# Optimization experiments

Hardware: AMD Instinct MI355X
Metric: run time of the kernel (lower is better)

Reference implementation:

```python
import jax, jax.numpy as jnp
import numpy as np

DIM = 1024
HEADS = 16
HEAD_DIM = DIM // HEADS
B, N = 4, 4096


def setup_inputs() -> dict:
    key = jax.random.key(0)
    ks = jax.random.split(key, 10)
    s = 1.0 / np.sqrt(DIM)
    return {
        "x": jax.random.normal(ks[0], (B, N, DIM), dtype=jnp.float32),
        "Wq": jax.random.uniform(ks[1], (DIM, DIM), jnp.float32, -s, s),
        "bq": jax.random.uniform(ks[2], (DIM,), jnp.float32, -s, s),
        "Wk": jax.random.uniform(ks[3], (DIM, DIM), jnp.float32, -s, s),
        "bk": jax.random.uniform(ks[4], (DIM,), jnp.float32, -s, s),
        "Wv": jax.random.uniform(ks[5], (DIM, DIM), jnp.float32, -s, s),
        "bv": jax.random.uniform(ks[6], (DIM,), jnp.float32, -s, s),
        "Wo": jax.random.uniform(ks[7], (DIM, DIM), jnp.float32, -s, s),
        "bo": jax.random.uniform(ks[8], (DIM,), jnp.float32, -s, s),
        "stdp": jnp.ones((HEADS,), dtype=jnp.float32),
    }


def reference(x, Wq, bq, Wk, bk, Wv, bv, Wo, bo, stdp):
    b, n, d = x.shape
    h, dh = HEADS, HEAD_DIM
    # projections (torch Linear: x @ W.T + b)
    def proj(W, bias):
        return (x @ W.T + bias).reshape(b, n, h, dh).transpose(0, 2, 1, 3)  # bhnd
    Q = jax.nn.elu(proj(Wq, bq)) + 1.0
    K = jax.nn.elu(proj(Wk, bk)) + 1.0
    V = proj(Wv, bv)
    stdp_w = jax.nn.sigmoid(stdp).reshape(1, h, 1, 1)
    KV = jnp.einsum('bhnd,bhnv->bhdv', K, V)      # (b,h,dh,dh)
    K_sum = K.sum(axis=2)                          # (b,h,dh)
    numerator = jnp.einsum('bhnd,bhdv->bhnv', Q, KV)
    denominator = jnp.einsum('bhnd,bhd->bhn', Q, K_sum)[..., None] + 1e-6
    attn_out = numerator / denominator * stdp_w    # (b,h,n,dh)
    out = attn_out.transpose(0, 2, 1, 3).reshape(b, n, d)
    out = out @ Wo.T + bo
    return (out, jax.lax.stop_gradient(stdp))
```

## Files before the change

### kernel.cpp

```cpp
#include <hip/hip_runtime.h>
#include <hip/hip_bf16.h>

#define DIMSZ 1024
#define SEQLEN 4096
#define NHEAD 16
#define NX 16777216L
#define NW 1048576L

typedef __attribute__((ext_vector_type(8))) short bf16x8;
typedef __attribute__((ext_vector_type(4))) float f32x4;

__device__ __forceinline__ unsigned short f2bf(float f) {
    union { float f; unsigned int i; } c; c.f = f;
    unsigned int x = c.i;
    unsigned int r = (x + 0x7fffu + ((x >> 16) & 1u)) >> 16;
    return (unsigned short)r;
}

__device__ __forceinline__ unsigned int pk2(float lo, float hi) {
    union { float f; unsigned int i; } a, b; a.f = lo; b.f = hi;
    return __builtin_amdgcn_perm(b.i + 0x8000u, a.i + 0x8000u, 0x07060302u);
}

__device__ __forceinline__ void unp8(const unsigned short* p, float* f) {
    uint4 w = *(const uint4*)p;
    union { unsigned int i; float f; } c;
    c.i = w.x << 16;           f[0] = c.f;
    c.i = w.x & 0xffff0000u;   f[1] = c.f;
    c.i = w.y << 16;           f[2] = c.f;
    c.i = w.y & 0xffff0000u;   f[3] = c.f;
    c.i = w.z << 16;           f[4] = c.f;
    c.i = w.z & 0xffff0000u;   f[5] = c.f;
    c.i = w.w << 16;           f[6] = c.f;
    c.i = w.w & 0xffff0000u;   f[7] = c.f;
}

__device__ __forceinline__ void unp8r(bf16x8 v, float* f) {
    union { bf16x8 s; uint4 w; } u; u.s = v;
    union { unsigned int i; float f; } c;
    c.i = u.w.x << 16;           f[0] = c.f;
    c.i = u.w.x & 0xffff0000u;   f[1] = c.f;
    c.i = u.w.y << 16;           f[2] = c.f;
    c.i = u.w.y & 0xffff0000u;   f[3] = c.f;
    c.i = u.w.z << 16;           f[4] = c.f;
    c.i = u.w.z & 0xffff0000u;   f[5] = c.f;
    c.i = u.w.w << 16;           f[6] = c.f;
    c.i = u.w.w & 0xffff0000u;   f[7] = c.f;
}

__device__ __forceinline__ void async16(const void* g, void* l) {
    __builtin_amdgcn_global_load_lds(
        (const __attribute__((address_space(1))) void*)g,
        (__attribute__((address_space(3))) void*)l,
        16, 0, 0);
}

__global__ __launch_bounds__(256) void cast_pack(
    const float* __restrict__ x, const float* __restrict__ Wq,
    const float* __restrict__ Wk, const float* __restrict__ Wv,
    const float* __restrict__ Wo, const float* __restrict__ stdp,
    unsigned short* __restrict__ xb, unsigned short* __restrict__ Wqkv,
    unsigned short* __restrict__ Wob, float* __restrict__ outTail)
{
    long i4 = ((long)blockIdx.x * 256 + threadIdx.x) * 4;
    const float* src; unsigned short* dst; long off;
    if (i4 < NX)               { src = x;  dst = xb;          off = i4; }
    else if (i4 < NX + NW)     { src = Wq; dst = Wqkv;        off = i4 - NX; }
    else if (i4 < NX + 2*NW)   { src = Wk; dst = Wqkv + NW;   off = i4 - NX - NW; }
    else if (i4 < NX + 3*NW)   { src = Wv; dst = Wqkv + 2*NW; off = i4 - NX - 2*NW; }
    else                       { src = Wo; dst = Wob;         off = i4 - NX - 3*NW; }
    float4 v = *(const float4*)(src + off);
    union { unsigned short u[4]; uint2 p; } o;
    o.u[0] = f2bf(v.x); o.u[1] = f2bf(v.y); o.u[2] = f2bf(v.z); o.u[3] = f2bf(v.w);
    *(uint2*)(dst + off) = o.p;
    if (blockIdx.x == 0 && threadIdx.x < NHEAD) outTail[threadIdx.x] = stdp[threadIdx.x];
}

__global__ __launch_bounds__(512, 2) void qkv_gemm8(
    const unsigned short* __restrict__ A, const unsigned short* __restrict__ W,
    const float* __restrict__ bq, const float* __restrict__ bk,
    const float* __restrict__ bv,
    unsigned short* __restrict__ Qb, unsigned short* __restrict__ Kb,
    unsigned short* __restrict__ Vb)
{
    __shared__ __align__(16) char SM[131072];
    const int t = threadIdx.x;
    const int wave = t >> 6, lane = t & 63;
    const int lr = lane & 15, lq = lane >> 4;
    const int wm = wave >> 2, wn = wave & 3;
    const int m0 = blockIdx.x * 256;
    const int c0 = blockIdx.y * 256;

    const int sc = (((t & 7) ^ ((t >> 3) & 7)) * 8);
    const unsigned short* pA = A + (long)(m0 + (t >> 3)) * DIMSZ + sc;
    const unsigned short* pB = W + (long)(c0 + (t >> 3)) * DIMSZ + sc;
    char* ldsW = SM + wave * 1024;

    const int xo = ((lq ^ (lr & 7)) << 4);
    const char* ABase = SM + wm * 16384 + lr * 128;
    const char* BBase = SM + 32768 + (wn * 64 + lr) * 128;

    f32x4 acc[8][4];
    #pragma unroll
    for (int i = 0; i < 8; ++i)
        #pragma unroll
        for (int j = 0; j < 4; ++j) acc[i][j] = (f32x4){0.f, 0.f, 0.f, 0.f};

#define STAGE(Q, O) do {                                                        \
        if ((Q) < 16) {                                                         \
            const int isB_ = ((O) < 2) ? 1 : 0;                                 \
            const int half_ = isB_ ? (O) : ((O) - 2);                           \
            const unsigned short* s_ = (isB_ ? pB : pA)                         \
                                       + (long)half_ * 131072 + (Q) * 64;       \
            char* d_ = ldsW + (((Q) & 1) << 16) + isB_ * 32768 + half_ * 16384; \
            async16(s_, d_);                                                    \
            async16(s_ + 65536, d_ + 8192);                                     \
        }                                                                       \
    } while (0)

    STAGE(0, 0); STAGE(0, 1); STAGE(0, 2); STAGE(0, 3);
    STAGE(1, 0); STAGE(1, 1); STAGE(1, 2);
    asm volatile("s_waitcnt vmcnt(6)" ::: "memory");
    __builtin_amdgcn_s_barrier();

    for (int kt = 0; kt < 16; ++kt) {
        const int buf = (kt & 1) << 16;
        bf16x8 a0[4][2], a1[4][2], bfr[4][2];

        #pragma unroll
        for (int j = 0; j < 4; ++j) {
            bfr[j][0] = *(const bf16x8*)(BBase + buf + j * 2048 + xo);
            bfr[j][1] = *(const bf16x8*)(BBase + buf + j * 2048 + (xo ^ 64));
        }
        #pragma unroll
        for (int i = 0; i < 4; ++i) {
            a0[i][0] = *(const bf16x8*)(ABase + buf + i * 2048 + xo);
            a0[i][1] = *(const bf16x8*)(ABase + buf + i * 2048 + (xo ^ 64));
        }
        STAGE(kt + 1, 3);
        __builtin_amdgcn_s_barrier();
        asm volatile("s_waitcnt lgkmcnt(0)" ::: "memory");
        __builtin_amdgcn_sched_barrier(0);
        __builtin_amdgcn_s_setprio(1);
        #pragma unroll
        for (int s = 0; s < 2; ++s)
            #pragma unroll
            for (int i = 0; i < 4; ++i)
                #pragma unroll
                for (int j = 0; j < 2; ++j)
                    acc[i][j] = __builtin_amdgcn_mfma_f32_16x16x32_bf16(
                        bfr[j][s], a0[i][s], acc[i][j], 0, 0, 0);
        __builtin_amdgcn_s_setprio(0);
        __builtin_amdgcn_s_barrier();

        STAGE(kt + 2, 0);
        __builtin_amdgcn_s_barrier();
        __builtin_amdgcn_s_setprio(1);
        #pragma unroll
        for (int s = 0; s < 2; ++s)
            #pragma unroll
            for (int i = 0; i < 4; ++i)
                #pragma unroll
                for (int j = 2; j < 4; ++j)
                    acc[i][j] = __builtin_amdgcn_mfma_f32_16x16x32_bf16(
                        bfr[j][s], a0[i][s], acc[i][j], 0, 0, 0);
        __builtin_amdgcn_s_setprio(0);
        __builtin_amdgcn_s_barrier();

        #pragma unroll
        for (int i = 0; i < 4; ++i) {
            a1[i][0] = *(const bf16x8*)(ABase + buf + (i + 4) * 2048 + xo);
            a1[i][1] = *(const bf16x8*)(ABase + buf + (i + 4) * 2048 + (xo ^ 64));
        }
        STAGE(kt + 2, 1);
        __builtin_amdgcn_s_barrier();
        asm volatile("s_waitcnt lgkmcnt(0)" ::: "memory");
        __builtin_amdgcn_sched_barrier(0);
        __builtin_amdgcn_s_setprio(1);
        #pragma unroll
        for (int s = 0; s < 2; ++s)
            #pragma unroll
            for (int i = 0; i < 4; ++i)
                #pragma unroll
                for (int j = 0; j < 2; ++j)
                    acc[i + 4][j] = __builtin_amdgcn_mfma_f32_16x16x32_bf16(
                        bfr[j][s], a1[i][s], acc[i + 4][j], 0, 0, 0);
        __builtin_amdgcn_s_setprio(0);
        __builtin_amdgcn_s_barrier();

        STAGE(kt + 2, 2);
        __builtin_amdgcn_s_barrier();
        __builtin_amdgcn_s_setprio(1);
        #pragma unroll
        for (int s = 0; s < 2; ++s)
            #pragma unroll
            for (int i = 0; i < 4; ++i)
                #pragma unroll
                for (int j = 2; j < 4; ++j)
                    acc[i + 4][j] = __builtin_amdgcn_mfma_f32_16x16x32_bf16(
                        bfr[j][s], a1[i][s], acc[i + 4][j], 0, 0, 0);
        __builtin_amdgcn_s_setprio(0);
        if (kt < 14)       asm volatile("s_waitcnt vmcnt(6)" ::: "memory");
        else if (kt == 14) asm volatile("s_waitcnt vmcnt(0)" ::: "memory");
        __builtin_amdgcn_s_barrier();
    }
#undef STAGE

    const int proj = c0 >> 10;
    const float* bias = proj == 0 ? bq : (proj == 1 ? bk : bv);
    const bool qk = proj < 2;
    const int cb = (c0 & 1023) + wn * 64;
    const int q4 = lq * 4;
    #pragma unroll
    for (int j = 0; j < 4; ++j) {
        const float4 b4 = *(const float4*)(bias + cb + 16 * j + q4);
        #pragma unroll
        for (int i = 0; i < 8; ++i) {
            float v0 = acc[i][j][0] + b4.x, v1 = acc[i][j][1] + b4.y;
            float v2 = acc[i][j][2] + b4.z, v3 = acc[i][j][3] + b4.w;
            if (qk) {
                v0 = v0 > 0.f ? v0 + 1.f : __expf(v0);
                v1 = v1 > 0.f ? v1 + 1.f : __expf(v1);
                v2 = v2 > 0.f ? v2 + 1.f : __expf(v2);
                v3 = v3 > 0.f ? v3 + 1.f : __expf(v3);
            }
            const int row = wm * 128 + 16 * i + lr;
            int byte = row * 512 + wn * 128 + j * 32 + q4 * 2;
            byte ^= (row & 7) << 4;
            uint2 pkd; pkd.x = pk2(v0, v1); pkd.y = pk2(v2, v3);
            *(uint2*)(SM + byte) = pkd;
        }
    }
    __syncthreads();
    unsigned short* dstp = proj == 0 ? Qb : (proj == 1 ? Kb : Vb);
    const int colsh = (t & 31) * 8;
    const int h = ((c0 >> 6) + (colsh >> 6)) & 15;
    const int b_ = m0 >> 12;
    unsigned short* dbase = dstp + ((long)(b_ * 16 + h) * SEQLEN) * 64 + (colsh & 63);
    #pragma unroll
    for (int u = 0; u < 16; ++u) {
        const int flat = u * 8192 + t * 16;
        const int row = flat >> 9;
        uint4 val = *(const uint4*)(SM + (flat ^ ((row & 7) << 4)));
        const int n = (m0 + row) & 4095;
        *(uint4*)(dbase + (long)n * 64) = val;
    }
}

__global__ __launch_bounds__(256) void kv_reduce(
    const unsigned short* __restrict__ Kb, const unsigned short* __restrict__ Vb,
    float* __restrict__ KVp, float* __restrict__ Ksump)
{
    __shared__ float red[4096];
    __shared__ float redk[64];
    int bh = blockIdx.x, split = blockIdx.y;
    int t = threadIdx.x;
    int dblk = t & 7, vblk = (t >> 3) & 7, nsub = t >> 6;
    int d0 = dblk * 8, v0 = vblk * 8;
    long rbase = ((long)bh * SEQLEN + split * 256 + nsub * 64) * 64;
    const unsigned short* Kp = Kb + rbase + d0;
    const unsigned short* Vp = Vb + rbase + v0;

    float acc[8][8];
    #pragma unroll
    for (int a = 0; a < 8; ++a)
        #pragma unroll
        for (int c = 0; c < 8; ++c) acc[a][c] = 0.f;
    float ks[8] = {0.f, 0.f, 0.f, 0.f, 0.f, 0.f, 0.f, 0.f};

    for (int i = 0; i < 64; ++i) {
        float kf[8], vf[8];
        unp8(Kp + (long)i * 64, kf);
        unp8(Vp + (long)i * 64, vf);
        if (vblk == 0) {
            #pragma unroll
            for (int d = 0; d < 8; ++d) ks[d] += kf[d];
        }
        #pragma unroll
        for (int vi = 0; vi < 8; ++vi)
            #pragma unroll
            for (int di = 0; di < 8; ++di) acc[vi][di] += vf[vi] * kf[di];
    }

    for (int p = 0; p < 4; ++p) {
        if (nsub == p) {
            #pragma unroll
            for (int vi = 0; vi < 8; ++vi)
                #pragma unroll
                for (int di = 0; di < 8; ++di) {
                    float* a = &red[(v0 + vi) * 64 + d0 + di];
                    if (p == 0) *a = acc[vi][di]; else *a += acc[vi][di];
                }
            if (vblk == 0) {
                #pragma unroll
                for (int di = 0; di < 8; ++di) {
                    float* a = &redk[d0 + di];
                    if (p == 0) *a = ks[di]; else *a += ks[di];
                }
            }
        }
        __syncthreads();
    }

    float* kp = KVp + ((long)split * 64 + bh) * 4096;
    #pragma unroll
    for (int u = 0; u < 4; ++u) {
        int idx = (u * 256 + t) * 4;
        *(float4*)(kp + idx) = *(const float4*)(red + idx);
    }
    if (t < 16)
        *(float4*)(Ksump + ((long)split * 64 + bh) * 64 + t * 4) = *(const float4*)(redk + t * 4);
}

__global__ __launch_bounds__(256) void kv_final(
    const float* __restrict__ KVp, const float* __restrict__ Ksump,
    unsigned short* __restrict__ KVb, float* __restrict__ Ksum)
{
    int bh = blockIdx.x, t = threadIdx.x;
    float s[16];
    #pragma unroll
    for (int g = 0; g < 16; ++g) s[g] = 0.f;
    for (int sp = 0; sp < 16; ++sp) {
        const float* src = KVp + ((long)sp * 64 + bh) * 4096 + t * 16;
        #pragma unroll
        for (int g = 0; g < 4; ++g) {
            float4 v = *(const float4*)(src + g * 4);
            s[g * 4 + 0] += v.x; s[g * 4 + 1] += v.y;
            s[g * 4 + 2] += v.z; s[g * 4 + 3] += v.w;
        }
    }
    uint4 o0, o1;
    o0.x = pk2(s[0], s[1]);  o0.y = pk2(s[2], s[3]);
    o0.z = pk2(s[4], s[5]);  o0.w = pk2(s[6], s[7]);
    o1.x = pk2(s[8], s[9]);  o1.y = pk2(s[10], s[11]);
    o1.z = pk2(s[12], s[13]); o1.w = pk2(s[14], s[15]);
    *(uint4*)(KVb + (long)bh * 4096 + t * 16) = o0;
    *(uint4*)(KVb + (long)bh * 4096 + t * 16 + 8) = o1;
    if (t < 16) {
        float4 a = {0.f, 0.f, 0.f, 0.f};
        for (int p = 0; p < 16; p += 4) {
            #pragma unroll
            for (int q = 0; q < 4; ++q) {
                float4 v = *(const float4*)(Ksump + ((long)(p + q) * 64 + bh) * 64 + t * 4);
                a.x += v.x; a.y += v.y; a.z += v.z; a.w += v.w;
            }
        }
        *(float4*)(Ksum + bh * 64 + t * 4) = a;
    }
}

__global__ __launch_bounds__(256) void attn_kernel(
    const unsigned short* __restrict__ Qb, const unsigned short* __restrict__ KVb,
    const float* __restrict__ Ksum, const float* __restrict__ stdp,
    unsigned short* __restrict__ attn)
{
    __shared__ unsigned short Cs[256 * 72];
    int t = threadIdx.x;
    int rc = blockIdx.x;
    int bh = blockIdx.y;
    int b = bh >> 4, h = bh & 15;

    int wave = t >> 6, lane = t & 63, lr = lane & 15, lk = (lane >> 4) * 8;
    int rowbase = rc * 256 + wave * 64;
    const unsigned short* kvb = KVb + (long)bh * 4096;
    const float* ksb = Ksum + bh * 64;

    f32x4 acc[4][4];
    #pragma unroll
    for (int i = 0; i < 4; ++i)
        #pragma unroll
        for (int j = 0; j < 4; ++j) acc[i][j] = (f32x4){0.f, 0.f, 0.f, 0.f};
    float ds[4] = {0.f, 0.f, 0.f, 0.f};

    #pragma unroll
    for (int s0 = 0; s0 < 64; s0 += 32) {
        bf16x8 af[4], bfr[4];
        #pragma unroll
        for (int i = 0; i < 4; ++i)
            af[i] = *(const bf16x8*)(Qb + ((long)bh * SEQLEN + rowbase + 16 * i + lr) * 64 + s0 + lk);
        #pragma unroll
        for (int j = 0; j < 4; ++j)
            bfr[j] = *(const bf16x8*)(kvb + (16 * j + lr) * 64 + s0 + lk);
        float4 ka = *(const float4*)(ksb + s0 + lk);
        float4 kb2 = *(const float4*)(ksb + s0 + lk + 4);
        float ksf[8] = {ka.x, ka.y, ka.z, ka.w, kb2.x, kb2.y, kb2.z, kb2.w};
        #pragma unroll
        for (int i = 0; i < 4; ++i) {
            float qf[8]; unp8r(af[i], qf);
            #pragma unroll
            for (int e = 0; e < 8; ++e) ds[i] += qf[e] * ksf[e];
        }
        #pragma unroll
        for (int i = 0; i < 4; ++i)
            #pragma unroll
            for (int j = 0; j < 4; ++j)
                acc[i][j] = __builtin_amdgcn_mfma_f32_16x16x32_bf16(bfr[j], af[i], acc[i][j], 0, 0, 0);
    }

    float sg = 1.f / (1.f + __expf(-stdp[h]));
    float dinv_i[4];
    #pragma unroll
    for (int i = 0; i < 4; ++i) {
        float d = ds[i];
        d += __shfl_xor(d, 16);
        d += __shfl_xor(d, 32);
        dinv_i[i] = sg / (d + 1e-6f);
    }

    int q4 = (lane >> 4) * 4;
    #pragma unroll
    for (int j = 0; j < 4; ++j) {
        int v0c = 16 * j + q4;
        #pragma unroll
        for (int i = 0; i < 4; ++i) {
            int row = wave * 64 + 16 * i + lr;
            float d = dinv_i[i];
            uint2 pkd;
            pkd.x = pk2(acc[i][j][0] * d, acc[i][j][1] * d);
            pkd.y = pk2(acc[i][j][2] * d, acc[i][j][3] * d);
            *(uint2*)(Cs + row * 72 + v0c) = pkd;
        }
    }
    __syncthreads();
    #pragma unroll
    for (int u = 0; u < 8; ++u) {
        int row = u * 32 + (t >> 3);
        int nn = rc * 256 + row;
        long a = ((long)(b * SEQLEN + nn)) * DIMSZ + h * 64 + (t & 7) * 8;
        *(uint4*)(attn + a) = *(const uint4*)(Cs + row * 72 + (t & 7) * 8);
    }
}

__global__ __launch_bounds__(512, 2) void out_gemm8(
    const unsigned short* __restrict__ A, const unsigned short* __restrict__ W,
    const float* __restrict__ bo, float* __restrict__ out)
{
    __shared__ __align__(16) char SM[131072];
    const int t = threadIdx.x;
    const int wave = t >> 6, lane = t & 63;
    const int lr = lane & 15, lq = lane >> 4;
    const int wm = wave >> 2, wn = wave & 3;
    const int m0 = blockIdx.x * 256;
    const int c0 = blockIdx.y * 256;

    const int sc = (((t & 7) ^ ((t >> 3) & 7)) * 8);
    const unsigned short* pA = A + (long)(m0 + (t >> 3)) * DIMSZ + sc;
    const unsigned short* pB = W + (long)(c0 + (t >> 3)) * DIMSZ + sc;
    char* ldsW = SM + wave * 1024;

    const int xo = ((lq ^ (lr & 7)) << 4);
    const char* ABase = SM + wm * 16384 + lr * 128;
    const char* BBase = SM + 32768 + (wn * 64 + lr) * 128;

    f32x4 acc[8][4];
    #pragma unroll
    for (int i = 0; i < 8; ++i)
        #pragma unroll
        for (int j = 0; j < 4; ++j) acc[i][j] = (f32x4){0.f, 0.f, 0.f, 0.f};

#define STAGE(Q, O) do {                                                        \
        if ((Q) < 16) {                                                         \
            const int isB_ = ((O) < 2) ? 1 : 0;                                 \
            const int half_ = isB_ ? (O) : ((O) - 2);                           \
            const unsigned short* s_ = (isB_ ? pB : pA)                         \
                                       + (long)half_ * 131072 + (Q) * 64;       \
            char* d_ = ldsW + (((Q) & 1) << 16) + isB_ * 32768 + half_ * 16384; \
            async16(s_, d_);                                                    \
            async16(s_ + 65536, d_ + 8192);                                     \
        }                                                                       \
    } while (0)

    STAGE(0, 0); STAGE(0, 1); STAGE(0, 2); STAGE(0, 3);
    STAGE(1, 0); STAGE(1, 1); STAGE(1, 2);
    asm volatile("s_waitcnt vmcnt(6)" ::: "memory");
    __builtin_amdgcn_s_barrier();

    for (int kt = 0; kt < 16; ++kt) {
        const int buf = (kt & 1) << 16;
        bf16x8 a0[4][2], a1[4][2], bfr[4][2];

        #pragma unroll
        for (int j = 0; j < 4; ++j) {
            bfr[j][0] = *(const bf16x8*)(BBase + buf + j * 2048 + xo);
            bfr[j][1] = *(const bf16x8*)(BBase + buf + j * 2048 + (xo ^ 64));
        }
        #pragma unroll
        for (int i = 0; i < 4; ++i) {
            a0[i][0] = *(const bf16x8*)(ABase + buf + i * 2048 + xo);
            a0[i][1] = *(const bf16x8*)(ABase + buf + i * 2048 + (xo ^ 64));
        }
        STAGE(kt + 1, 3);
        __builtin_amdgcn_s_barrier();
        asm volatile("s_waitcnt lgkmcnt(0)" ::: "memory");
        __builtin_amdgcn_sched_barrier(0);
        __builtin_amdgcn_s_setprio(1);
        #pragma unroll
        for (int s = 0; s < 2; ++s)
            #pragma unroll
            for (int i = 0; i < 4; ++i)
                #pragma unroll
                for (int j = 0; j < 2; ++j)
                    acc[i][j] = __builtin_amdgcn_mfma_f32_16x16x32_bf16(
                        bfr[j][s], a0[i][s], acc[i][j], 0, 0, 0);
        __builtin_amdgcn_s_setprio(0);
        __builtin_amdgcn_s_barrier();

        STAGE(kt + 2, 0);
        __builtin_amdgcn_s_barrier();
        __builtin_amdgcn_s_setprio(1);
        #pragma unroll
        for (int s = 0; s < 2; ++s)
            #pragma unroll
            for (int i = 0; i < 4; ++i)
                #pragma unroll
                for (int j = 2; j < 4; ++j)
                    acc[i][j] = __builtin_amdgcn_mfma_f32_16x16x32_bf16(
                        bfr[j][s], a0[i][s], acc[i][j], 0, 0, 0);
        __builtin_amdgcn_s_setprio(0);
        __builtin_amdgcn_s_barrier();

        #pragma unroll
        for (int i = 0; i < 4; ++i) {
            a1[i][0] = *(const bf16x8*)(ABase + buf + (i + 4) * 2048 + xo);
            a1[i][1] = *(const bf16x8*)(ABase + buf + (i + 4) * 2048 + (xo ^ 64));
        }
        STAGE(kt + 2, 1);
        __builtin_amdgcn_s_barrier();
        asm volatile("s_waitcnt lgkmcnt(0)" ::: "memory");
        __builtin_amdgcn_sched_barrier(0);
        __builtin_amdgcn_s_setprio(1);
        #pragma unroll
        for (int s = 0; s < 2; ++s)
            #pragma unroll
            for (int i = 0; i < 4; ++i)
                #pragma unroll
                for (int j = 0; j < 2; ++j)
                    acc[i + 4][j] = __builtin_amdgcn_mfma_f32_16x16x32_bf16(
                        bfr[j][s], a1[i][s], acc[i + 4][j], 0, 0, 0);
        __builtin_amdgcn_s_setprio(0);
        __builtin_amdgcn_s_barrier();

        STAGE(kt + 2, 2);
        __builtin_amdgcn_s_barrier();
        __builtin_amdgcn_s_setprio(1);
        #pragma unroll
        for (int s = 0; s < 2; ++s)
            #pragma unroll
            for (int i = 0; i < 4; ++i)
                #pragma unroll
                for (int j = 2; j < 4; ++j)
                    acc[i + 4][j] = __builtin_amdgcn_mfma_f32_16x16x32_bf16(
                        bfr[j][s], a1[i][s], acc[i + 4][j], 0, 0, 0);
        __builtin_amdgcn_s_setprio(0);
        if (kt < 14)       asm volatile("s_waitcnt vmcnt(6)" ::: "memory");
        else if (kt == 14) asm volatile("s_waitcnt vmcnt(0)" ::: "memory");
        __builtin_amdgcn_s_barrier();
    }
#undef STAGE

    const int q4 = lq * 4;
    #pragma unroll
    for (int j = 0; j < 4; ++j) {
        const int c = c0 + wn * 64 + 16 * j + q4;
        const float4 b4 = *(const float4*)(bo + c);
        #pragma unroll
        for (int i = 0; i < 8; ++i) {
            const int gm = m0 + wm * 128 + 16 * i + lr;
            float4 v;
            v.x = acc[i][j][0] + b4.x; v.y = acc[i][j][1] + b4.y;
            v.z = acc[i][j][2] + b4.z; v.w = acc[i][j][3] + b4.w;
            *(float4*)(out + (long)gm * DIMSZ + c) = v;
        }
    }
}

extern "C" void kernel_launch(void* const* d_in, const int* in_sizes, int n_in,
                              void* d_out, int out_size, void* d_ws, size_t ws_size,
                              hipStream_t stream) {
    const float* x    = (const float*)d_in[0];
    const float* Wq   = (const float*)d_in[1];
    const float* bq   = (const float*)d_in[2];
    const float* Wk   = (const float*)d_in[3];
    const float* bk   = (const float*)d_in[4];
    const float* Wv   = (const float*)d_in[5];
    const float* bv   = (const float*)d_in[6];
    const float* Wo   = (const float*)d_in[7];
    const float* bo   = (const float*)d_in[8];
    const float* stdp = (const float*)d_in[9];
    float* out = (float*)d_out;

    char* ws = (char*)d_ws;
    unsigned short* xb   = (unsigned short*)(ws);
    float*          KVp  = (float*)(ws);
    unsigned short* attn = (unsigned short*)(ws);
    unsigned short* Wqkv = (unsigned short*)(ws + 33554432L);
    float*          Ksump= (float*)(ws + 33554432L);
    unsigned short* KVb  = (unsigned short*)(ws + 33816576L);
    float*          Ksum = (float*)(ws + 34340864L);
    unsigned short* Wob  = (unsigned short*)(ws + 39845888L);
    unsigned short* Qb   = (unsigned short*)(ws + 41943040L);
    unsigned short* Kb   = (unsigned short*)(ws + 75497472L);
    unsigned short* Vb   = (unsigned short*)(ws + 109051904L);

    cast_pack<<<20480, 256, 0, stream>>>(x, Wq, Wk, Wv, Wo, stdp, xb, Wqkv, Wob,
                                         out + 16777216L);
    qkv_gemm8<<<dim3(64, 12), 512, 0, stream>>>(xb, Wqkv, bq, bk, bv, Qb, Kb, Vb);
    kv_reduce<<<dim3(64, 16), 256, 0, stream>>>(Kb, Vb, KVp, Ksump);
    kv_final<<<64, 256, 0, stream>>>(KVp, Ksump, KVb, Ksum);
    attn_kernel<<<dim3(16, 64), 256, 0, stream>>>(Qb, KVb, Ksum, stdp, attn);
    out_gemm8<<<dim3(64, 4), 512, 0, stream>>>(attn, Wob, bo, out);
}
```

Before: 345.7 us.

## Use MFMA for KV reduction and split B-fragment loads in GEMM pipeline

The kv_reduce kernel is rewritten to stage K and V tiles, transposed and swizzled, into LDS and then compute K^T V with bf16 MFMA instructions. This replaces the scalar FMA outer-product loop and the serialized four-pass shared-memory reduction. In both GEMM kernels, the B-fragment LDS reads are split into two halves, and the global staging calls are re-sequenced so that fewer register fragments are live at once. This reshuffles the memory/compute interleaving and adds an extra lgkmcnt wait.

Result: faster. 323.8 us (-6.4%).

```diff
diff --git a/kernel.cpp b/kernel.cpp
--- a/kernel.cpp
+++ b/kernel.cpp
@@ -20,19 +20,6 @@
 __device__ __forceinline__ unsigned int pk2(float lo, float hi) {
     union { float f; unsigned int i; } a, b; a.f = lo; b.f = hi;
     return __builtin_amdgcn_perm(b.i + 0x8000u, a.i + 0x8000u, 0x07060302u);
-}
-
-__device__ __forceinline__ void unp8(const unsigned short* p, float* f) {
-    uint4 w = *(const uint4*)p;
-    union { unsigned int i; float f; } c;
-    c.i = w.x << 16;           f[0] = c.f;
-    c.i = w.x & 0xffff0000u;   f[1] = c.f;
-    c.i = w.y << 16;           f[2] = c.f;
-    c.i = w.y & 0xffff0000u;   f[3] = c.f;
-    c.i = w.z << 16;           f[4] = c.f;
-    c.i = w.z & 0xffff0000u;   f[5] = c.f;
-    c.i = w.w << 16;           f[6] = c.f;
-    c.i = w.w & 0xffff0000u;   f[7] = c.f;
 }
 
 __device__ __forceinline__ void unp8r(bf16x8 v, float* f) {
@@ -128,7 +115,7 @@
         bf16x8 a0[4][2], a1[4][2], bfr[4][2];
 
         #pragma unroll
-        for (int j = 0; j < 4; ++j) {
+        for (int j = 0; j < 2; ++j) {
             bfr[j][0] = *(const bf16x8*)(BBase + buf + j * 2048 + xo);
             bfr[j][1] = *(const bf16x8*)(BBase + buf + j * 2048 + (xo ^ 64));
         }
@@ -153,8 +140,14 @@
         __builtin_amdgcn_s_setprio(0);
         __builtin_amdgcn_s_barrier();
 
-        STAGE(kt + 2, 0);
-        __builtin_amdgcn_s_barrier();
+        #pragma unroll
+        for (int j = 2; j < 4; ++j) {
+            bfr[j][0] = *(const bf16x8*)(BBase + buf + j * 2048 + xo);
+            bfr[j][1] = *(const bf16x8*)(BBase + buf + j * 2048 + (xo ^ 64));
+        }
+        __builtin_amdgcn_s_barrier();
+        asm volatile("s_waitcnt lgkmcnt(0)" ::: "memory");
+        __builtin_amdgcn_sched_barrier(0);
         __builtin_amdgcn_s_setprio(1);
         #pragma unroll
         for (int s = 0; s < 2; ++s)
@@ -172,7 +165,7 @@
             a1[i][0] = *(const bf16x8*)(ABase + buf + (i + 4) * 2048 + xo);
             a1[i][1] = *(const bf16x8*)(ABase + buf + (i + 4) * 2048 + (xo ^ 64));
         }
-        STAGE(kt + 2, 1);
+        STAGE(kt + 2, 0);
         __builtin_amdgcn_s_barrier();
         asm volatile("s_waitcnt lgkmcnt(0)" ::: "memory");
         __builtin_amdgcn_sched_barrier(0);
@@ -188,6 +181,7 @@
         __builtin_amdgcn_s_setprio(0);
         __builtin_amdgcn_s_barrier();
 
+        STAGE(kt + 2, 1);
         STAGE(kt + 2, 2);
         __builtin_amdgcn_s_barrier();
         __builtin_amdgcn_s_setprio(1);
@@ -251,65 +245,88 @@
     const unsigned short* __restrict__ Kb, const unsigned short* __restrict__ Vb,
     float* __restrict__ KVp, float* __restrict__ Ksump)
 {
-    __shared__ float red[4096];
-    __shared__ float redk[64];
-    int bh = blockIdx.x, split = blockIdx.y;
-    int t = threadIdx.x;
-    int dblk = t & 7, vblk = (t >> 3) & 7, nsub = t >> 6;
-    int d0 = dblk * 8, v0 = vblk * 8;
-    long rbase = ((long)bh * SEQLEN + split * 256 + nsub * 64) * 64;
-    const unsigned short* Kp = Kb + rbase + d0;
-    const unsigned short* Vp = Vb + rbase + v0;
-
-    float acc[8][8];
-    #pragma unroll
-    for (int a = 0; a < 8; ++a)
-        #pragma unroll
-        for (int c = 0; c < 8; ++c) acc[a][c] = 0.f;
-    float ks[8] = {0.f, 0.f, 0.f, 0.f, 0.f, 0.f, 0.f, 0.f};
-
-    for (int i = 0; i < 64; ++i) {
-        float kf[8], vf[8];
-        unp8(Kp + (long)i * 64, kf);
-        unp8(Vp + (long)i * 64, vf);
-        if (vblk == 0) {
-            #pragma unroll
-            for (int d = 0; d < 8; ++d) ks[d] += kf[d];
-        }
-        #pragma unroll
-        for (int vi = 0; vi < 8; ++vi)
-            #pragma unroll
-            for (int di = 0; di < 8; ++di) acc[vi][di] += vf[vi] * kf[di];
-    }
-
-    for (int p = 0; p < 4; ++p) {
-        if (nsub == p) {
-            #pragma unroll
-            for (int vi = 0; vi < 8; ++vi)
-                #pragma unroll
-                for (int di = 0; di < 8; ++di) {
-                    float* a = &red[(v0 + vi) * 64 + d0 + di];
-                    if (p == 0) *a = acc[vi][di]; else *a += acc[vi][di];
-                }
-            if (vblk == 0) {
-                #pragma unroll
-                for (int di = 0; di < 8; ++di) {
-                    float* a = &redk[d0 + di];
-                    if (p == 0) *a = ks[di]; else *a += ks[di];
+    __shared__ __align__(16) char LDS[65536];
+    int bh = blockIdx.x, split = blockIdx.y, t = threadIdx.x;
+    int wave = t >> 6, lane = t & 63, lr = lane & 15, lq = lane >> 4;
+
+    const unsigned short* Kbase = Kb + ((long)bh * SEQLEN + split * 256) * 64;
+    const unsigned short* Vbase = Vb + ((long)bh * SEQLEN + split * 256) * 64;
+
+    const int nl = t & 127;
+    const int dh = (t >> 7) * 32;
+
+    union Q2S { uint4 q[4]; unsigned short s[32]; };
+    Q2S kq[2], vq[2];
+    #pragma unroll
+    for (int it = 0; it < 2; ++it) {
+        const unsigned short* kp = Kbase + (long)(it * 128 + nl) * 64 + dh;
+        const unsigned short* vp = Vbase + (long)(it * 128 + nl) * 64 + dh;
+        #pragma unroll
+        for (int g = 0; g < 4; ++g) {
+            kq[it].q[g] = *(const uint4*)(kp + g * 8);
+            vq[it].q[g] = *(const uint4*)(vp + g * 8);
+        }
+    }
+    #pragma unroll
+    for (int it = 0; it < 2; ++it) {
+        char* buf = LDS + it * 32768;
+        #pragma unroll
+        for (int e = 0; e < 32; ++e) {
+            const int d = dh + e;
+            const int a = d * 256 + ((nl * 2) ^ ((d & 7) << 4));
+            *(unsigned short*)(buf + a) = kq[it].s[e];
+            *(unsigned short*)(buf + 16384 + a) = vq[it].s[e];
+        }
+    }
+    __syncthreads();
+
+    f32x4 acc[4];
+    #pragma unroll
+    for (int j = 0; j < 4; ++j) acc[j] = (f32x4){0.f, 0.f, 0.f, 0.f};
+    float ksp[4] = {0.f, 0.f, 0.f, 0.f};
+
+    const int vrow = 16 * wave + lr;
+    #pragma unroll
+    for (int it = 0; it < 2; ++it) {
+        const char* buf = LDS + it * 32768;
+        #pragma unroll
+        for (int ns = 0; ns < 4; ++ns) {
+            const int xoff = (ns * 64 + lq * 16) ^ ((lr & 7) << 4);
+            bf16x8 af = *(const bf16x8*)(buf + 16384 + vrow * 256 + xoff);
+            bf16x8 bfr[4];
+            #pragma unroll
+            for (int j = 0; j < 4; ++j)
+                bfr[j] = *(const bf16x8*)(buf + (16 * j + lr) * 256 + xoff);
+            if (wave == 0) {
+                #pragma unroll
+                for (int j = 0; j < 4; ++j) {
+                    float kf[8]; unp8r(bfr[j], kf);
+                    ksp[j] += ((kf[0] + kf[1]) + (kf[2] + kf[3]))
+                            + ((kf[4] + kf[5]) + (kf[6] + kf[7]));
                 }
             }
-        }
-        __syncthreads();
+            #pragma unroll
+            for (int j = 0; j < 4; ++j)
+                acc[j] = __builtin_amdgcn_mfma_f32_16x16x32_bf16(bfr[j], af, acc[j], 0, 0, 0);
+        }
     }
 
     float* kp = KVp + ((long)split * 64 + bh) * 4096;
-    #pragma unroll
-    for (int u = 0; u < 4; ++u) {
-        int idx = (u * 256 + t) * 4;
-        *(float4*)(kp + idx) = *(const float4*)(red + idx);
-    }
-    if (t < 16)
-        *(float4*)(Ksump + ((long)split * 64 + bh) * 64 + t * 4) = *(const float4*)(redk + t * 4);
+    const int q4 = lq * 4;
+    #pragma unroll
+    for (int j = 0; j < 4; ++j)
+        *(f32x4*)(kp + vrow * 64 + 16 * j + q4) = acc[j];
+
+    if (wave == 0) {
+        #pragma unroll
+        for (int j = 0; j < 4; ++j) {
+            float s = ksp[j];
+            s += __shfl_xor(s, 16);
+            s += __shfl_xor(s, 32);
+            if (lane < 16)
+                Ksump[((long)split * 64 + bh) * 64 + 16 * j + lr] = s;
+        }
+    }
 }
 
 __global__ __launch_bounds__(256) void kv_final(
@@ -480,7 +497,7 @@
         bf16x8 a0[4][2], a1[4][2], bfr[4][2];
 
         #pragma unroll
-        for (int j = 0; j < 4; ++j) {
+        for (int j = 0; j < 2; ++j) {
             bfr[j][0] = *(const bf16x8*)(BBase + buf + j * 2048 + xo);
             bfr[j][1] = *(const bf16x8*)(BBase + buf + j * 2048 + (xo ^ 64));
         }
@@ -505,8 +522,14 @@
         __builtin_amdgcn_s_setprio(0);
         __builtin_amdgcn_s_barrier();
 
-        STAGE(kt + 2, 0);
-        __builtin_amdgcn_s_barrier();
+        #pragma unroll
+        for (int j = 2; j < 4; ++j) {
+            bfr[j][0] = *(const bf16x8*)(BBase + buf + j * 2048 + xo);
+            bfr[j][1] = *(const bf16x8*)(BBase + buf + j * 2048 + (xo ^ 64));
+        }
+        __builtin_amdgcn_s_barrier();
+        asm volatile("s_waitcnt lgkmcnt(0)" ::: "memory");
+        __builtin_amdgcn_sched_barrier(0);
         __builtin_amdgcn_s_setprio(1);
         #pragma unroll
         for (int s = 0; s < 2; ++s)
@@ -524,7 +547,7 @@
             a1[i][0] = *(const bf16x8*)(ABase + buf + (i + 4) * 2048 + xo);
             a1[i][1] = *(const bf16x8*)(ABase + buf + (i + 4) * 2048 + (xo ^ 64));
         }
-        STAGE(kt + 2, 1);
+        STAGE(kt + 2, 0);
         __builtin_amdgcn_s_barrier();
         asm volatile("s_waitcnt lgkmcnt(0)" ::: "memory");
         __builtin_amdgcn_sched_barrier(0);
@@ -540,6 +563,7 @@
         __builtin_amdgcn_s_setprio(0);
         __builtin_amdgcn_s_barrier();
 
+        STAGE(kt + 2, 1);
         STAGE(kt + 2, 2);
         __builtin_amdgcn_s_barrier();
         __builtin_amdgcn_s_setprio(1);
```
